# Optimization experiments

Measured on AMD Instinct MI355X. Metric: run time of the kernel, lower is better.

The kernel has to match this reference:

```python
import jax, jax.numpy as jnp
import numpy as np

# Dims (match init_kwargs)
B, S, D = 2, 2048, 2048
H = 16
Q_LORA, KV_LORA = 768, 512
NOPE, ROPE, VD = 128, 64, 128
QHD = NOPE + ROPE  # 192


def setup_inputs() -> dict:
    key = jax.random.key(0)
    ks = jax.random.split(key, 7)
    w = lambda k, shape: (jax.random.normal(k, shape, jnp.float32) * 0.02)
    return {
        "x": jax.random.normal(ks[0], (B, S, D), jnp.float32),
        "position": jnp.broadcast_to(jnp.arange(S, dtype=jnp.int32), (B, S)),
        "mask": jnp.tril(jnp.ones((1, 1, S, S), jnp.int32)),  # causal
        "w_q_down": w(ks[1], (D, Q_LORA)),                 # (in, out) layout
        "w_q_up": w(ks[2], (Q_LORA, H * QHD)),
        "w_kv_down": w(ks[3], (D, KV_LORA + ROPE)),
        "w_kv_up": w(ks[4], (KV_LORA, H * (NOPE + VD))),
        "w_out": w(ks[5], (H * VD, D)),
    }


def reference(x, position, mask, w_q_down, w_q_up, w_kv_down, w_kv_up, w_out):
    # position unused: rope_embedding is None in the source module.
    # Low-rank Q: down then up projection.
    q = (x @ w_q_down) @ w_q_up                      # [B,S,H*QHD]
    q = q.reshape(B, S, H, QHD).transpose(0, 2, 1, 3)  # [B,H,S,QHD]
    q_nope, q_rope = q[..., :NOPE], q[..., NOPE:]

    # Low-rank KV: down projection yields compressed kv + shared rope key.
    c = x @ w_kv_down                                # [B,S,KV_LORA+ROPE]
    c_kv, k_rope = c[..., :KV_LORA], c[..., KV_LORA:]
    k_rope = k_rope[:, None, :, :]                   # [B,1,S,ROPE]

    kv = (c_kv @ w_kv_up).reshape(B, S, H, NOPE + VD).transpose(0, 2, 1, 3)
    k_nope, v = kv[..., :NOPE], kv[..., NOPE:]       # [B,H,S,NOPE], [B,H,S,VD]

    q_state = jnp.concatenate([q_nope, q_rope], axis=-1)           # [B,H,S,QHD]
    k_state = jnp.concatenate(
        [k_nope, jnp.broadcast_to(k_rope, (B, H, S, ROPE))], axis=-1)

    scale = 1.0 / jnp.sqrt(jnp.float32(VD))  # source divides by sqrt(v_head_dim)
    scores = jnp.einsum("bhqd,bhkd->bhqk", q_state, k_state) * scale
    scores = jnp.where(mask == 0, jnp.float32(-jnp.inf), scores)
    att = jax.nn.softmax(scores, axis=-1)            # dropout_rate=0 (eval)
    out = jnp.einsum("bhqk,bhkd->bhqd", att, v)      # [B,H,S,VD]
    out = out.transpose(0, 2, 1, 3).reshape(B, S, H * VD)
    return out @ w_out
```

## Files before the change

### kernel.cpp

```cpp
#include <hip/hip_runtime.h>

typedef __bf16 bf16;
typedef bf16 bf16x8 __attribute__((ext_vector_type(8)));
typedef bf16 bf16x4 __attribute__((ext_vector_type(4)));
typedef float f32x4 __attribute__((ext_vector_type(4)));
typedef short s16x4 __attribute__((ext_vector_type(4)));

#define AS1 __attribute__((address_space(1)))
#define AS3 __attribute__((address_space(3)))

__device__ __forceinline__ void load_lds16(const void* g, void* l) {
    __builtin_amdgcn_global_load_lds((const AS1 unsigned int*)g,
                                     (AS3 unsigned int*)l, 16, 0, 0);
}

__global__ __launch_bounds__(256) void cast_f32_bf16(
        const float* __restrict__ in, bf16* __restrict__ out, int n) {
    int i = (blockIdx.x * 256 + threadIdx.x) * 4;
    if (i < n) {
        float4 v = *(const float4*)(in + i);
        bf16x4 o = { (bf16)v.x, (bf16)v.y, (bf16)v.z, (bf16)v.w };
        *(bf16x4*)(out + i) = o;
    }
}

__global__ __launch_bounds__(256) void transpose_cast(
        const float* __restrict__ in, bf16* __restrict__ out,
        int K, int N, int Np) {
    __shared__ float tile[32][33];
    int bx = blockIdx.x * 32;
    int by = blockIdx.y * 32;
    int tx = threadIdx.x, ty = threadIdx.y;
#pragma unroll
    for (int i = 0; i < 4; ++i) {
        int k = by + ty + i * 8, n = bx + tx;
        float v = (k < K && n < N) ? in[(size_t)k * N + n] : 0.f;
        tile[ty + i * 8][tx] = v;
    }
    __syncthreads();
#pragma unroll
    for (int i = 0; i < 4; ++i) {
        int n = bx + ty + i * 8, k = by + tx;
        if (n < Np && k < K) out[(size_t)n * K + k] = (bf16)tile[tx][ty + i * 8];
    }
}

__global__ __launch_bounds__(256) void transpose_v(
        const bf16* __restrict__ kvb, bf16* __restrict__ vtb) {
    __shared__ bf16 t[32][34];
    const int kv0 = blockIdx.x * 32;
    const int vd0 = blockIdx.y * 32;
    const int bh = blockIdx.z;
    const int b = bh >> 4, h = bh & 15;
    const int tx = threadIdx.x, ty = threadIdx.y;
#pragma unroll
    for (int i = 0; i < 4; ++i)
        t[ty + i * 8][tx] = kvb[(size_t)(b * 2048 + kv0 + ty + i * 8) * 4096
                                + h * 256 + 128 + vd0 + tx];
    __syncthreads();
#pragma unroll
    for (int i = 0; i < 4; ++i)
        vtb[(size_t)(bh * 128 + vd0 + ty + i * 8) * 2048 + kv0 + tx] =
            t[tx][ty + i * 8];
}

template <typename OutT>
__global__ __launch_bounds__(256) void gemm_bt(
        const bf16* __restrict__ A, const bf16* __restrict__ Bt,
        OutT* __restrict__ C, int K, int lda, int ldb, int ldc) {
    __shared__ __align__(16) bf16 As[128 * 64];
    __shared__ __align__(16) bf16 Bs[128 * 64];
    const int tid = threadIdx.x;
    const int wave = tid >> 6, lane = tid & 63;
    const int l15 = lane & 15, quad = lane >> 4;
    const int m0 = blockIdx.y * 128, n0 = blockIdx.x * 128;
    const int wm = (wave >> 1) * 64, wn = (wave & 1) * 64;

    f32x4 acc[4][4] = {};

    for (int k0 = 0; k0 < K; k0 += 64) {
#pragma unroll
        for (int c = 0; c < 4; ++c) {
            int e = wave * 2048 + c * 512 + lane * 8;
            int r = e >> 6, col = e & 63;
            load_lds16(A + (size_t)(m0 + r) * lda + k0 + col,
                       &As[wave * 2048 + c * 512]);
            load_lds16(Bt + (size_t)(n0 + r) * ldb + k0 + col,
                       &Bs[wave * 2048 + c * 512]);
        }
        __syncthreads();
#pragma unroll
        for (int kk = 0; kk < 64; kk += 32) {
            bf16x8 af[4], bf[4];
#pragma unroll
            for (int i = 0; i < 4; ++i)
                af[i] = *(const bf16x8*)&As[(wm + i * 16 + l15) * 64 + kk + quad * 8];
#pragma unroll
            for (int j = 0; j < 4; ++j)
                bf[j] = *(const bf16x8*)&Bs[(wn + j * 16 + l15) * 64 + kk + quad * 8];
#pragma unroll
            for (int i = 0; i < 4; ++i)
#pragma unroll
                for (int j = 0; j < 4; ++j)
                    acc[i][j] = __builtin_amdgcn_mfma_f32_16x16x32_bf16(
                        af[i], bf[j], acc[i][j], 0, 0, 0);
        }
        __syncthreads();
    }
#pragma unroll
    for (int i = 0; i < 4; ++i)
#pragma unroll
        for (int j = 0; j < 4; ++j) {
            int row = m0 + wm + i * 16 + quad * 4;
            int col = n0 + wn + j * 16 + l15;
#pragma unroll
            for (int r = 0; r < 4; ++r)
                C[(size_t)(row + r) * ldc + col] = (OutT)acc[i][j][r];
        }
}

__global__ __launch_bounds__(256) void gemm_down(
        const bf16* __restrict__ A, const bf16* __restrict__ Bt,
        bf16* __restrict__ C1, bf16* __restrict__ C2) {
    const int K = 2048, lda = 2048, ldb = 2048;
    __shared__ __align__(16) bf16 As[128 * 64];
    __shared__ __align__(16) bf16 Bs[128 * 64];
    const int tid = threadIdx.x;
    const int wave = tid >> 6, lane = tid & 63;
    const int l15 = lane & 15, quad = lane >> 4;
    const int m0 = blockIdx.y * 128, n0 = blockIdx.x * 128;
    const int wm = (wave >> 1) * 64, wn = (wave & 1) * 64;

    f32x4 acc[4][4] = {};

    for (int k0 = 0; k0 < K; k0 += 64) {
#pragma unroll
        for (int c = 0; c < 4; ++c) {
            int e = wave * 2048 + c * 512 + lane * 8;
            int r = e >> 6, col = e & 63;
            load_lds16(A + (size_t)(m0 + r) * lda + k0 + col,
                       &As[wave * 2048 + c * 512]);
            load_lds16(Bt + (size_t)(n0 + r) * ldb + k0 + col,
                       &Bs[wave * 2048 + c * 512]);
        }
        __syncthreads();
#pragma unroll
        for (int kk = 0; kk < 64; kk += 32) {
            bf16x8 af[4], bf[4];
#pragma unroll
            for (int i = 0; i < 4; ++i)
                af[i] = *(const bf16x8*)&As[(wm + i * 16 + l15) * 64 + kk + quad * 8];
#pragma unroll
            for (int j = 0; j < 4; ++j)
                bf[j] = *(const bf16x8*)&Bs[(wn + j * 16 + l15) * 64 + kk + quad * 8];
#pragma unroll
            for (int i = 0; i < 4; ++i)
#pragma unroll
                for (int j = 0; j < 4; ++j)
                    acc[i][j] = __builtin_amdgcn_mfma_f32_16x16x32_bf16(
                        af[i], bf[j], acc[i][j], 0, 0, 0);
        }
        __syncthreads();
    }
    bf16* Cp; int ldc, coff;
    if (n0 < 768) { Cp = C1; ldc = 768; coff = 0; }
    else          { Cp = C2; ldc = 640; coff = 768; }
#pragma unroll
    for (int i = 0; i < 4; ++i)
#pragma unroll
        for (int j = 0; j < 4; ++j) {
            int row = m0 + wm + i * 16 + quad * 4;
            int col = n0 + wn + j * 16 + l15 - coff;
#pragma unroll
            for (int r = 0; r < 4; ++r)
                Cp[(size_t)(row + r) * ldc + col] = (bf16)acc[i][j][r];
        }
}

__global__ __launch_bounds__(512, 4) void mla_attention_split(
        const bf16* __restrict__ qb, const bf16* __restrict__ kvb,
        const bf16* __restrict__ cb, const bf16* __restrict__ vtb,
        bf16* __restrict__ ob, bf16* __restrict__ part_o,
        float* __restrict__ part_ml) {
    constexpr int S = 2048;
    const int idx = 23 - blockIdx.x;
    const int h = blockIdx.y, b = blockIdx.z;
    int qt, t0, t1, c;
    if (idx < 8) { qt = idx; t0 = 0; t1 = 2 * qt + 2; c = -1; }
    else {
        qt = 8 + ((idx - 8) >> 1);
        c = (idx - 8) & 1;
        if (c == 0) { t0 = 0;  t1 = 16; }
        else        { t0 = 16; t1 = 2 * qt + 2; }
    }
    const int q0 = qt * 128;
    const int tid = threadIdx.x, wave = tid >> 6, lane = tid & 63;
    const int l15 = lane & 15, quad = lane >> 4;

    __shared__ __align__(16) bf16 Ks[2][24 * 512];
    __shared__ __align__(16) bf16 Vs[2][8 * 1024];

    const int qrow = q0 + wave * 16 + l15;
    bf16x8 qf[6];
    {
        const bf16* qr = qb + (size_t)(b * S + qrow) * 3072 + h * 192;
#pragma unroll
        for (int ks = 0; ks < 6; ++ks)
            qf[ks] = *(const bf16x8*)(qr + ks * 32 + quad * 8);
    }

    const bf16* vt_head = vtb + (size_t)((b * 16 + h) * 128) * 2048;

    auto stage = [&](int kt, int bufi) {
        const int kv0 = kt * 64;
        const int mt = wave >> 1;
        const size_t row = (size_t)(b * S + kv0 + mt * 16 + l15);
#pragma unroll
        for (int i = 0; i < 3; ++i) {
            const int ks = (wave & 1) * 3 + i;
            const bf16* g = (ks < 4)
                ? kvb + row * 4096 + h * 256 + ks * 32 + quad * 8
                : cb  + row * 640  + 512 + (ks - 4) * 32 + quad * 8;
            load_lds16(g, &Ks[bufi][(mt * 6 + ks) * 512]);
        }
#pragma unroll
        for (int i = 0; i < 2; ++i) {
            const bf16* g = vt_head + (size_t)(wave * 16 + l15) * 2048
                            + kv0 + (i * 4 + quad) * 8;
            load_lds16(g, &Vs[bufi][wave * 1024 + i * 512]);
        }
    };

    f32x4 o[8] = {};
    float m_i = -1e30f, l_i = 0.f;
    const float sm_scale = 0.08838834764831845f * 1.4426950408889634f;
    const int qmin_w = q0 + wave * 16;

    stage(t0, 0);
    stage(t0 + 1, 1);

    int cur = 0;
    for (int kt = t0; kt < t1; ++kt, cur ^= 1) {
        const int kv0 = kt * 64;

        if (kt + 1 < t1) asm volatile("s_waitcnt vmcnt(5)" ::: "memory");
        else             asm volatile("s_waitcnt vmcnt(0)" ::: "memory");
        __builtin_amdgcn_s_barrier();
        __builtin_amdgcn_sched_barrier(0);

        f32x4 s[4];
        __builtin_amdgcn_s_setprio(1);
#pragma unroll
        for (int mt = 0; mt < 4; ++mt) {
            f32x4 a = {};
#pragma unroll
            for (int ks = 0; ks < 6; ++ks) {
                bf16x8 kf = *(const bf16x8*)&Ks[cur][(mt * 6 + ks) * 512 + lane * 8];
                a = __builtin_amdgcn_mfma_f32_16x16x32_bf16(kf, qf[ks], a, 0, 0, 0);
            }
            s[mt] = a;
        }
        __builtin_amdgcn_s_setprio(0);

        if (kv0 + 63 > qmin_w) {
#pragma unroll
            for (int mt = 0; mt < 4; ++mt)
#pragma unroll
                for (int r = 0; r < 4; ++r) {
                    int kvi = kv0 + mt * 16 + quad * 4 + r;
                    s[mt][r] = (kvi <= qrow) ? s[mt][r] * sm_scale : -1e30f;
                }
        } else {
#pragma unroll
            for (int mt = 0; mt < 4; ++mt)
#pragma unroll
                for (int r = 0; r < 4; ++r)
                    s[mt][r] = s[mt][r] * sm_scale;
        }
        float mx4[4];
#pragma unroll
        for (int mt = 0; mt < 4; ++mt)
            mx4[mt] = fmaxf(fmaxf(s[mt][0], s[mt][1]),
                            fmaxf(s[mt][2], s[mt][3]));
        float mx = fmaxf(fmaxf(mx4[0], mx4[1]), fmaxf(mx4[2], mx4[3]));
        mx = fmaxf(mx, __shfl_xor(mx, 16, 64));
        mx = fmaxf(mx, __shfl_xor(mx, 32, 64));
        float m_new = fmaxf(m_i, mx);
        float su4[4];
        bf16x4 pf[4];
#pragma unroll
        for (int mt = 0; mt < 4; ++mt) {
            float e0 = exp2f(s[mt][0] - m_new);
            float e1 = exp2f(s[mt][1] - m_new);
            float e2 = exp2f(s[mt][2] - m_new);
            float e3 = exp2f(s[mt][3] - m_new);
            su4[mt] = (e0 + e1) + (e2 + e3);
            pf[mt][0] = (bf16)e0; pf[mt][1] = (bf16)e1;
            pf[mt][2] = (bf16)e2; pf[mt][3] = (bf16)e3;
        }
        float su = (su4[0] + su4[1]) + (su4[2] + su4[3]);
        su += __shfl_xor(su, 16, 64);
        su += __shfl_xor(su, 32, 64);
        if (__all(mx <= m_i)) {
            l_i += su;
        } else {
            float alpha = exp2f(m_i - m_new);
            l_i = l_i * alpha + su;
            m_i = m_new;
            float alpha_r[4];
#pragma unroll
            for (int r = 0; r < 4; ++r)
                alpha_r[r] = __shfl(alpha, quad * 4 + r, 64);
#pragma unroll
            for (int nt = 0; nt < 8; ++nt)
#pragma unroll
                for (int r = 0; r < 4; ++r) o[nt][r] *= alpha_r[r];
        }

        __builtin_amdgcn_s_setprio(1);
#pragma unroll
        for (int ktk = 0; ktk < 4; ++ktk) {
            s16x4 a = __builtin_bit_cast(s16x4, pf[ktk]);
            const int voff = ktk * 256 + (quad >> 1) * 128 + l15 * 8 + (quad & 1) * 4;
#pragma unroll
            for (int nt = 0; nt < 8; ++nt) {
                s16x4 bfv = __builtin_bit_cast(s16x4,
                    *(const bf16x4*)&Vs[cur][nt * 1024 + voff]);
                o[nt] = __builtin_amdgcn_mfma_f32_16x16x16bf16_1k(a, bfv, o[nt], 0, 0, 0);
            }
        }
        __builtin_amdgcn_s_setprio(0);

        __builtin_amdgcn_s_barrier();
        if (kt + 2 < t1) stage(kt + 2, cur);
    }

    if (c < 0) {
        float l_r[4];
#pragma unroll
        for (int r = 0; r < 4; ++r) l_r[r] = __shfl(l_i, quad * 4 + r, 64);
        bf16* obase = ob + (size_t)(b * S + q0 + wave * 16) * 2048 + h * 128;
#pragma unroll
        for (int nt = 0; nt < 8; ++nt)
#pragma unroll
            for (int r = 0; r < 4; ++r)
                obase[(size_t)(quad * 4 + r) * 2048 + nt * 16 + l15] =
                    (bf16)(o[nt][r] / l_r[r]);
    } else {
        const int slot = (b * 16 + h) * 8 + (qt - 8);
        if (quad == 0) {
            const int qlocal = wave * 16 + l15;
            part_ml[(slot * 2 + c) * 256 + qlocal] = m_i;
            part_ml[(slot * 2 + c) * 256 + 128 + qlocal] = l_i;
        }
        if (c == 0) {
            bf16* pb = part_o + (size_t)slot * 16384
                       + (size_t)(wave * 16) * 128;
#pragma unroll
            for (int nt = 0; nt < 8; ++nt)
#pragma unroll
                for (int r = 0; r < 4; ++r)
                    pb[(quad * 4 + r) * 128 + nt * 16 + l15] = (bf16)o[nt][r];
        } else {
            bf16* obase = ob + (size_t)(b * S + q0 + wave * 16) * 2048 + h * 128;
#pragma unroll
            for (int nt = 0; nt < 8; ++nt)
#pragma unroll
                for (int r = 0; r < 4; ++r)
                    obase[(size_t)(quad * 4 + r) * 2048 + nt * 16 + l15] =
                        (bf16)o[nt][r];
        }
    }
}

__global__ __launch_bounds__(256) void mla_merge(
        const bf16* __restrict__ part_o, const float* __restrict__ part_ml,
        bf16* __restrict__ ob) {
    const int qt = 8 + blockIdx.x, h = blockIdx.y, b = blockIdx.z;
    const int slot = (b * 16 + h) * 8 + (qt - 8);
    const int tid = threadIdx.x;
    const int row = tid >> 1;
    const int col = (tid & 1) * 64;
    const float* ml0 = part_ml + (size_t)(slot * 2) * 256;
    const float* ml1 = ml0 + 256;
    const float m0 = ml0[row], l0v = ml0[128 + row];
    const float m1 = ml1[row], l1v = ml1[128 + row];
    const float M = fmaxf(m0, m1);
    float a0 = exp2f(m0 - M), a1 = exp2f(m1 - M);
    const float inv = 1.f / (l0v * a0 + l1v * a1);
    a0 *= inv; a1 *= inv;
    const bf16* p0 = part_o + (size_t)slot * 16384 + row * 128 + col;
    bf16* po = ob + (size_t)(b * 2048 + qt * 128 + row) * 2048 + h * 128 + col;
#pragma unroll
    for (int i = 0; i < 8; ++i) {
        bf16x8 v0 = *(const bf16x8*)(p0 + i * 8);
        bf16x8 v1 = *(const bf16x8*)(po + i * 8);
        bf16x8 om;
#pragma unroll
        for (int u = 0; u < 8; ++u)
            om[u] = (bf16)((float)v0[u] * a0 + (float)v1[u] * a1);
        *(bf16x8*)(po + i * 8) = om;
    }
}

extern "C" void kernel_launch(void* const* d_in, const int* in_sizes, int n_in,
                              void* d_out, int out_size, void* d_ws, size_t ws_size,
                              hipStream_t stream) {
    const float* x    = (const float*)d_in[0];
    const float* wqd  = (const float*)d_in[3];
    const float* wqu  = (const float*)d_in[4];
    const float* wkvd = (const float*)d_in[5];
    const float* wkvu = (const float*)d_in[6];
    const float* wout = (const float*)d_in[7];
    float* out = (float*)d_out;
    char* ws = (char*)d_ws;

    bf16* xb    = (bf16*)(ws + 0);
    bf16* vtb   = (bf16*)(ws + 0);
    bf16* wqdT  = (bf16*)(ws + 16777216);
    bf16* wkvdT = (bf16*)(ws + 19922944);
    bf16* wquT  = (bf16*)(ws + 22544384);
    bf16* wkvuT = (bf16*)(ws + 27262976);
    bf16* part_o  = (bf16*)(ws + 16777216);
    float* part_ml = (float*)(ws + 25165824);
    bf16* woutT = (bf16*)(ws + 31457280);
    bf16* qd    = (bf16*)(ws + 39845888);
    bf16* qb    = (bf16*)(ws + 46137344);
    bf16* cb    = (bf16*)(ws + 71303168);
    bf16* kvb   = (bf16*)(ws + 76546048);
    bf16* attnb = (bf16*)(ws + 110100480);

    dim3 tb(32, 8);
    cast_f32_bf16<<<8192, 256, 0, stream>>>(x, xb, 8388608);
    transpose_cast<<<dim3(24, 64),  tb, 0, stream>>>(wqd,  wqdT,  2048, 768,  768);
    transpose_cast<<<dim3(20, 64),  tb, 0, stream>>>(wkvd, wkvdT, 2048, 576,  640);
    transpose_cast<<<dim3(96, 24),  tb, 0, stream>>>(wqu,  wquT,  768,  3072, 3072);
    transpose_cast<<<dim3(128, 16), tb, 0, stream>>>(wkvu, wkvuT, 512,  4096, 4096);
    transpose_cast<<<dim3(64, 64),  tb, 0, stream>>>(wout, woutT, 2048, 2048, 2048);

    gemm_down<<<dim3(11, 32), 256, 0, stream>>>(xb, wqdT, qd, cb);
    gemm_bt<bf16><<<dim3(24, 32), 256, 0, stream>>>(qd, wquT,  qb,  768, 768, 768, 3072);
    gemm_bt<bf16><<<dim3(32, 32), 256, 0, stream>>>(cb, wkvuT, kvb, 512, 640, 512, 4096);

    transpose_v<<<dim3(64, 4, 32), tb, 0, stream>>>(kvb, vtb);

    mla_attention_split<<<dim3(24, 16, 2), 512, 0, stream>>>(
        qb, kvb, cb, vtb, attnb, part_o, part_ml);
    mla_merge<<<dim3(8, 16, 2), 256, 0, stream>>>(part_o, part_ml, attnb);

    gemm_bt<float><<<dim3(16, 32), 256, 0, stream>>>(attnb, woutT, out, 2048, 2048, 2048, 2048);
}
```

Before: 472.0 us.

## Use 256-row query tiles with 16 waves and variable KV split-count balancing

```diff
diff --git a/kernel.cpp b/kernel.cpp
--- a/kernel.cpp
+++ b/kernel.cpp
@@ -177,23 +177,24 @@
         }
 }
 
-__global__ __launch_bounds__(512, 4) void mla_attention_split(
+__global__ __launch_bounds__(1024, 8) void mla_attention_split(
         const bf16* __restrict__ qb, const bf16* __restrict__ kvb,
         const bf16* __restrict__ cb, const bf16* __restrict__ vtb,
         bf16* __restrict__ ob, bf16* __restrict__ part_o,
         float* __restrict__ part_ml) {
     constexpr int S = 2048;
-    const int idx = 23 - blockIdx.x;
+    const signed char k_of[20]  = {7,7,7,7, 6,6,6,6, 5,5,5, 4,4,4, 3,3, 2,2, 1, 0};
+    const signed char c_of[20]  = {0,1,2,3, 0,1,2,3, 0,1,2, 0,1,2, 0,1, 0,1, 0, 0};
+    const signed char np_of[8]  = {1,1,2,2,3,3,4,4};
+    const signed char pre_of[8] = {0,0,0,1,2,4,6,9};
+
+    const int k  = k_of[blockIdx.x], c = c_of[blockIdx.x];
+    const int np = np_of[k];
     const int h = blockIdx.y, b = blockIdx.z;
-    int qt, t0, t1, c;
-    if (idx < 8) { qt = idx; t0 = 0; t1 = 2 * qt + 2; c = -1; }
-    else {
-        qt = 8 + ((idx - 8) >> 1);
-        c = (idx - 8) & 1;
-        if (c == 0) { t0 = 0;  t1 = 16; }
-        else        { t0 = 16; t1 = 2 * qt + 2; }
-    }
-    const int q0 = qt * 128;
+    const int T  = 4 * k + 4;
+    const int t0 = (c * T) / np, t1 = ((c + 1) * T) / np;
+    const int q0 = k * 256;
+
     const int tid = threadIdx.x, wave = tid >> 6, lane = tid & 63;
     const int l15 = lane & 15, quad = lane >> 4;
 
@@ -213,21 +214,25 @@
 
     auto stage = [&](int kt, int bufi) {
         const int kv0 = kt * 64;
-        const int mt = wave >> 1;
-        const size_t row = (size_t)(b * S + kv0 + mt * 16 + l15);
-#pragma unroll
-        for (int i = 0; i < 3; ++i) {
-            const int ks = (wave & 1) * 3 + i;
-            const bf16* g = (ks < 4)
-                ? kvb + row * 4096 + h * 256 + ks * 32 + quad * 8
-                : cb  + row * 640  + 512 + (ks - 4) * 32 + quad * 8;
-            load_lds16(g, &Ks[bufi][(mt * 6 + ks) * 512]);
-        }
-#pragma unroll
-        for (int i = 0; i < 2; ++i) {
-            const bf16* g = vt_head + (size_t)(wave * 16 + l15) * 2048
-                            + kv0 + (i * 4 + quad) * 8;
-            load_lds16(g, &Vs[bufi][wave * 1024 + i * 512]);
+        if (wave < 8) {
+            const int mt = wave >> 1;
+            const size_t row = (size_t)(b * S + kv0 + mt * 16 + l15);
+#pragma unroll
+            for (int i = 0; i < 3; ++i) {
+                const int ks = (wave & 1) * 3 + i;
+                const bf16* g = (ks < 4)
+                    ? kvb + row * 4096 + h * 256 + ks * 32 + quad * 8
+                    : cb  + row * 640  + 512 + (ks - 4) * 32 + quad * 8;
+                load_lds16(g, &Ks[bufi][(mt * 6 + ks) * 512]);
+            }
+        } else {
+            const int nt = wave - 8;
+#pragma unroll
+            for (int i = 0; i < 2; ++i) {
+                const bf16* g = vt_head + (size_t)(nt * 16 + l15) * 2048
+                                + kv0 + (i * 4 + quad) * 8;
+                load_lds16(g, &Vs[bufi][nt * 1024 + i * 512]);
+            }
         }
     };
 
@@ -243,8 +248,12 @@
     for (int kt = t0; kt < t1; ++kt, cur ^= 1) {
         const int kv0 = kt * 64;
 
-        if (kt + 1 < t1) asm volatile("s_waitcnt vmcnt(5)" ::: "memory");
-        else             asm volatile("s_waitcnt vmcnt(0)" ::: "memory");
+        if (kt + 1 < t1) {
+            if (wave < 8) asm volatile("s_waitcnt vmcnt(3)" ::: "memory");
+            else          asm volatile("s_waitcnt vmcnt(2)" ::: "memory");
+        } else {
+            asm volatile("s_waitcnt vmcnt(0)" ::: "memory");
+        }
         __builtin_amdgcn_s_barrier();
         __builtin_amdgcn_sched_barrier(0);
 
@@ -335,7 +344,7 @@
         if (kt + 2 < t1) stage(kt + 2, cur);
     }
 
-    if (c < 0) {
+    if (np == 1) {
         float l_r[4];
 #pragma unroll
         for (int r = 0; r < 4; ++r) l_r[r] = __shfl(l_i, quad * 4 + r, 64);
@@ -347,21 +356,14 @@
                 obase[(size_t)(quad * 4 + r) * 2048 + nt * 16 + l15] =
                     (bf16)(o[nt][r] / l_r[r]);
     } else {
-        const int slot = (b * 16 + h) * 8 + (qt - 8);
+        const int bh = b * 16 + h;
         if (quad == 0) {
             const int qlocal = wave * 16 + l15;
-            part_ml[(slot * 2 + c) * 256 + qlocal] = m_i;
-            part_ml[(slot * 2 + c) * 256 + 128 + qlocal] = l_i;
-        }
-        if (c == 0) {
-            bf16* pb = part_o + (size_t)slot * 16384
-                       + (size_t)(wave * 16) * 128;
-#pragma unroll
-            for (int nt = 0; nt < 8; ++nt)
-#pragma unroll
-                for (int r = 0; r < 4; ++r)
-                    pb[(quad * 4 + r) * 128 + nt * 16 + l15] = (bf16)o[nt][r];
-        } else {
+            float* mlp = part_ml + ((size_t)(bh * 8 + k) * 4 + c) * 512;
+            mlp[qlocal] = m_i;
+            mlp[256 + qlocal] = l_i;
+        }
+        if (c == np - 1) {
             bf16* obase = ob + (size_t)(b * S + q0 + wave * 16) * 2048 + h * 128;
 #pragma unroll
             for (int nt = 0; nt < 8; ++nt)
@@ -369,6 +371,14 @@
                 for (int r = 0; r < 4; ++r)
                     obase[(size_t)(quad * 4 + r) * 2048 + nt * 16 + l15] =
                         (bf16)o[nt][r];
+        } else {
+            bf16* pb = part_o + (size_t)(bh * 12 + pre_of[k] + c) * 32768
+                       + (size_t)(wave * 16) * 128;
+#pragma unroll
+            for (int nt = 0; nt < 8; ++nt)
+#pragma unroll
+                for (int r = 0; r < 4; ++r)
+                    pb[(quad * 4 + r) * 128 + nt * 16 + l15] = (bf16)o[nt][r];
         }
     }
 }
@@ -376,29 +386,53 @@
 __global__ __launch_bounds__(256) void mla_merge(
         const bf16* __restrict__ part_o, const float* __restrict__ part_ml,
         bf16* __restrict__ ob) {
-    const int qt = 8 + blockIdx.x, h = blockIdx.y, b = blockIdx.z;
-    const int slot = (b * 16 + h) * 8 + (qt - 8);
-    const int tid = threadIdx.x;
-    const int row = tid >> 1;
-    const int col = (tid & 1) * 64;
-    const float* ml0 = part_ml + (size_t)(slot * 2) * 256;
-    const float* ml1 = ml0 + 256;
-    const float m0 = ml0[row], l0v = ml0[128 + row];
-    const float m1 = ml1[row], l1v = ml1[128 + row];
-    const float M = fmaxf(m0, m1);
+    const signed char np_of[8]  = {1,1,2,2,3,3,4,4};
+    const signed char pre_of[8] = {0,0,0,1,2,4,6,9};
+    const int k = 2 + blockIdx.x;
+    const int h = blockIdx.y, b = blockIdx.z;
+    const int bh = b * 16 + h;
+    const int np = np_of[k];
+    const int row = threadIdx.x;
+
+    const float* mlb = part_ml + (size_t)(bh * 8 + k) * 4 * 512;
+    const float m0 = mlb[row],            l0 = mlb[256 + row];
+    const float m1 = mlb[512 + row],      l1 = mlb[512 + 256 + row];
+    const float m2 = (np > 2) ? mlb[1024 + row] : -1e30f;
+    const float l2 = (np > 2) ? mlb[1024 + 256 + row] : 0.f;
+    const float m3 = (np > 3) ? mlb[1536 + row] : -1e30f;
+    const float l3 = (np > 3) ? mlb[1536 + 256 + row] : 0.f;
+    const float M = fmaxf(fmaxf(m0, m1), fmaxf(m2, m3));
     float a0 = exp2f(m0 - M), a1 = exp2f(m1 - M);
-    const float inv = 1.f / (l0v * a0 + l1v * a1);
-    a0 *= inv; a1 *= inv;
-    const bf16* p0 = part_o + (size_t)slot * 16384 + row * 128 + col;
-    bf16* po = ob + (size_t)(b * 2048 + qt * 128 + row) * 2048 + h * 128 + col;
-#pragma unroll
-    for (int i = 0; i < 8; ++i) {
+    float a2 = exp2f(m2 - M), a3 = exp2f(m3 - M);
+    const float inv = 1.f / (l0 * a0 + l1 * a1 + l2 * a2 + l3 * a3);
+    a0 *= inv; a1 *= inv; a2 *= inv; a3 *= inv;
+    const float alast = (np == 2) ? a1 : (np == 3) ? a2 : a3;
+
+    const bf16* p0 = part_o + (size_t)(bh * 12 + pre_of[k]) * 32768 + row * 128;
+    const bf16* p1 = p0 + 32768;
+    const bf16* p2 = p1 + 32768;
+    bf16* po = ob + (size_t)(b * 2048 + k * 256 + row) * 2048 + h * 128;
+#pragma unroll
+    for (int i = 0; i < 16; ++i) {
+        bf16x8 vb = *(const bf16x8*)(po + i * 8);
         bf16x8 v0 = *(const bf16x8*)(p0 + i * 8);
-        bf16x8 v1 = *(const bf16x8*)(po + i * 8);
+        float acc[8];
+#pragma unroll
+        for (int u = 0; u < 8; ++u)
+            acc[u] = (float)vb[u] * alast + (float)v0[u] * a0;
+        if (np > 2) {
+            bf16x8 v1 = *(const bf16x8*)(p1 + i * 8);
+#pragma unroll
+            for (int u = 0; u < 8; ++u) acc[u] += (float)v1[u] * a1;
+        }
+        if (np > 3) {
+            bf16x8 v2 = *(const bf16x8*)(p2 + i * 8);
+#pragma unroll
+            for (int u = 0; u < 8; ++u) acc[u] += (float)v2[u] * a2;
+        }
         bf16x8 om;
 #pragma unroll
-        for (int u = 0; u < 8; ++u)
-            om[u] = (bf16)((float)v0[u] * a0 + (float)v1[u] * a1);
+        for (int u = 0; u < 8; ++u) om[u] = (bf16)acc[u];
         *(bf16x8*)(po + i * 8) = om;
     }
 }
@@ -421,8 +455,8 @@
     bf16* wkvdT = (bf16*)(ws + 19922944);
     bf16* wquT  = (bf16*)(ws + 22544384);
     bf16* wkvuT = (bf16*)(ws + 27262976);
-    bf16* part_o  = (bf16*)(ws + 16777216);
-    float* part_ml = (float*)(ws + 25165824);
+    float* part_ml = (float*)(ws + 16777216);
+    bf16* part_o  = (bf16*)out;
     bf16* woutT = (bf16*)(ws + 31457280);
     bf16* qd    = (bf16*)(ws + 39845888);
     bf16* qb    = (bf16*)(ws + 46137344);
@@ -444,9 +478,9 @@
 
     transpose_v<<<dim3(64, 4, 32), tb, 0, stream>>>(kvb, vtb);
 
-    mla_attention_split<<<dim3(24, 16, 2), 512, 0, stream>>>(
+    mla_attention_split<<<dim3(20, 16, 2), 1024, 0, stream>>>(
         qb, kvb, cb, vtb, attnb, part_o, part_ml);
-    mla_merge<<<dim3(8, 16, 2), 256, 0, stream>>>(part_o, part_ml, attnb);
+    mla_merge<<<dim3(6, 16, 2), 256, 0, stream>>>(part_o, part_ml, attnb);
 
     gemm_bt<float><<<dim3(16, 32), 256, 0, stream>>>(attnb, woutT, out, 2048, 2048, 2048, 2048);
 }
```

Result: slower. 708.3 us (+50.1%).
